# Kernel tuning notes

Hardware: AMD Instinct MI355X
Metric: run time of the kernel (lower is better)

Reference implementation:

```python
import jax, jax.numpy as jnp
import numpy as np

# task -> non-background class ids, padded with -1 to fixed width 3
NBG = np.array([[0, 1, 2], [0, 3, 4], [0, 5, 6], [0, 7, 8],
                [0, 9, -1], [0, 10, -1], [0, 11, -1]], dtype=np.int32)
NEG = -1e9      # pad logit (finite stand-in for -inf, grad-safe)
SMOOTH = 1e-5
NUM_CLASSES = 12


def setup_inputs() -> dict:
    key = jax.random.key(0)
    k1, k2, k3 = jax.random.split(key, 3)
    B, C, D, H, W = 4, 12, 32, 128, 128
    inputs = jax.random.normal(k1, (B, C, D, H, W), dtype=jnp.float32)
    task_id = jax.random.randint(k2, (B,), 0, 7, dtype=jnp.int32)
    # build targets consistent with each sample's task: labels in task_nbg[task]
    raw = jax.random.randint(k3, (B, D, H, W), 0, 3, dtype=jnp.int32)
    nbg = jnp.asarray(NBG)
    ids = nbg[task_id]                                   # [B,3]
    valid_max = jnp.where(ids[:, 2] < 0, 1, 2)           # 2-class tasks: raw in {0,1}
    raw = jnp.minimum(raw, valid_max[:, None, None, None])
    targets = jnp.take_along_axis(ids, raw.reshape(B, -1), axis=1).reshape(B, D, H, W)
    return {"inputs": inputs, "targets": targets, "task_id": task_id}


def reference(inputs, targets, task_id):
    B = inputs.shape[0]
    probs = jax.nn.softmax(inputs, axis=1)               # [B,12,D,H,W]
    nbg = jnp.asarray(NBG)
    ids = nbg[task_id]                                   # [B,3]
    mask = (ids >= 0)                                    # [B,3]
    idsc = jnp.maximum(ids, 0)
    mask5 = mask[:, :, None, None, None]
    gathered = jnp.take_along_axis(probs, idsc[:, :, None, None, None], axis=1)  # [B,3,D,H,W]
    score = jnp.where(mask5, gathered, 0.0)

    # --- remapped marginal targets: labels > 0 shifted by delta ---
    t = task_id.astype(jnp.int32)
    delta = jnp.where(t <= 4, -2 * t, -t - 4)
    tm = jnp.where(targets > 0, targets + delta[:, None, None, None], targets)   # in {0,1,2}

    # --- marginal CE: log_softmax over gathered probs (note: probs, not logits, matching torch F.cross_entropy on softmaxed inputs) ---
    logits = jnp.where(mask5, gathered, NEG)
    logp = jax.nn.log_softmax(logits, axis=1)
    nll = -jnp.take_along_axis(logp, tm[:, None], axis=1)[:, 0]                  # [B,D,H,W]
    loss_marg_ce = nll.mean(axis=(1, 2, 3)).sum() / B

    # --- marginal dice (padded classes contribute exactly 0) ---
    tgt = ((targets[:, None] == idsc[:, :, None, None, None]) & mask5).astype(probs.dtype)
    inter = jnp.sum(score * tgt, axis=(2, 3, 4))
    y_sum = jnp.sum(tgt, axis=(2, 3, 4))                 # tgt is binary: tgt*tgt == tgt
    z_sum = jnp.sum(score * score, axis=(2, 3, 4))
    dice = (2 * inter + SMOOTH) / (z_sum + y_sum + SMOOTH)
    loss_marg_dice = (1.0 - dice).sum() / B

    # --- exclusion: target_e = 1 - onehot(targets, 0..11), class 0 zeroed ---
    cls = jnp.arange(NUM_CLASSES, dtype=targets.dtype)[None, :, None, None, None]
    onehot = (targets[:, None] == cls).astype(probs.dtype)
    te = 1.0 - onehot
    te = te.at[:, 0].set(0.0)
    inter_e = jnp.sum(probs * te, axis=(2, 3, 4))
    y_e = jnp.sum(te, axis=(2, 3, 4))
    z_e = jnp.sum(probs * probs, axis=(2, 3, 4))
    dice_e = (2 * inter_e + SMOOTH) / (z_e + y_e + SMOOTH)
    loss_exc_dice = dice_e.sum() / B                     # inv=True: sum of dice scores

    loss_exc_ce = (jnp.log1p(probs) * te).mean(axis=(2, 3, 4)).sum() / B

    return (loss_marg_dice, loss_marg_ce, loss_exc_dice, loss_exc_ce)
```

## Files before the change

kernel.cpp:

```cpp
#include <hip/hip_runtime.h>


#define S2 262144
#define BLOCKS_PER_B 512
#define THREADS 256
#define ITERS 2
#define NVOX 524288.0f
#define SMOOTH 1e-5f

#define WRED(v) { v += __shfl_down(v,32); v += __shfl_down(v,16); \
                  v += __shfl_down(v,8);  v += __shfl_down(v,4);  \
                  v += __shfl_down(v,2);  v += __shfl_down(v,1); }

#define PROC2(X, TG, COMP) do {                                                \
  float xv[12];                                                                \
  _Pragma("unroll")                                                            \
  for (int c = 0; c < 12; ++c) xv[c] = X[c].COMP;                              \
  const int tgt = TG.COMP;                                                     \
  float m = xv[0];                                                             \
  _Pragma("unroll")                                                            \
  for (int c = 1; c < 12; ++c) m = fmaxf(m, xv[c]);                            \
  float e[12]; float es = 0.f;                                                 \
  _Pragma("unroll")                                                            \
  for (int c = 0; c < 12; ++c) { e[c] = __expf(xv[c] - m); es += e[c]; }       \
  const float r = __builtin_amdgcn_rcpf(es);                                   \
  float p[12];                                                                 \
  _Pragma("unroll")                                                            \
  for (int c = 0; c < 12; ++c) {                                               \
    p[c] = e[c] * r;                                                           \
    aZ[c] += p[c] * p[c];                                                      \
    aP[c] += p[c];                                                             \
  }                                                                            \
  float q = 1.f;                                                               \
  _Pragma("unroll")                                                            \
  for (int c = 1; c < 12; ++c) q = __builtin_fmaf(p[c], q, q);                 \
  const float g0 = p[0];                                                       \
  float g1 = 0.f, g2 = 0.f;                                                    \
  _Pragma("unroll")                                                            \
  for (int c = 1; c < 12; ++c) {                                               \
    if (c==1||c==3||c==5||c==7||c==9||c==10||c==11) g1 = (id1==c) ? p[c] : g1; \
    else                                            g2 = (id2==c) ? p[c] : g2; \
  }                                                                            \
  const bool t0 = (tgt == 0);                                                  \
  const bool t1 = (tgt == id1);                                                \
  const bool t2 = (tgt == id2);                                                \
  c0 += t0 ? 1.f : 0.f;  c1 += t1 ? 1.f : 0.f;  c2 += t2 ? 1.f : 0.f;          \
  p0S += t0 ? g0 : 0.f;  p1S += t1 ? g1 : 0.f;  p2S += t2 ? g2 : 0.f;          \
  const float pt = t1 ? g1 : (t2 ? g2 : 0.f);                                  \
  cesE += __logf(q * __builtin_amdgcn_rcpf(1.f + pt));                         \
  float s3 = __expf(g0) + __expf(g1);                                          \
  if (v2) s3 += __expf(g2);                                                    \
  const float gt = t0 ? g0 : (t1 ? g1 : g2);                                   \
  ces += __logf(s3) - gt;                                                      \
} while (0)

__global__ void zero_acc(float* __restrict__ acc) {
  acc[threadIdx.x] = 0.f;
}

__global__ __launch_bounds__(THREADS, 4)
void marg_main(const float2* __restrict__ inp, const int2* __restrict__ tgtp,
               const int* __restrict__ task_id, float* __restrict__ acc) {
  const int b   = blockIdx.x / BLOCKS_PER_B;
  const int blk = blockIdx.x % BLOCKS_PER_B;
  const int t   = task_id[b];
  const int id1 = (t <= 4) ? 2*t + 1 : t + 5;
  const int id2 = (t <= 3) ? 2*t + 2 : -1;
  const bool v2 = (id2 >= 0);

  const float2* inB = inp  + (size_t)b * 12 * S2;
  const int2*   tgB = tgtp + (size_t)b * S2;

  float aZ[12], aP[12];
  #pragma unroll
  for (int c = 0; c < 12; ++c) { aZ[c]=0.f; aP[c]=0.f; }
  float ces=0.f, cesE=0.f, c0=0.f, c1=0.f, c2=0.f, p0S=0.f, p1S=0.f, p2S=0.f;

  #pragma unroll 1
  for (int it = 0; it < ITERS; ++it) {
    const int s = blk * (ITERS * THREADS) + it * THREADS + (int)threadIdx.x;
    float2 x[12];
    #pragma unroll
    for (int c = 0; c < 12; ++c) x[c] = inB[c * S2 + s];
    const int2 tg = tgB[s];
    PROC2(x, tg, x); PROC2(x, tg, y);
  }

  WRED(ces); WRED(cesE); WRED(c0); WRED(c1); WRED(c2);
  WRED(p0S); WRED(p1S); WRED(p2S);
  #pragma unroll
  for (int c = 0; c < 12; ++c) { WRED(aZ[c]); WRED(aP[c]); }

  __shared__ float red[4][32];
  const int lane = threadIdx.x & 63;
  const int wv   = threadIdx.x >> 6;
  if (lane == 0) {
    float* rw = red[wv];
    rw[0]=ces; rw[1]=cesE; rw[2]=c0; rw[3]=c1; rw[4]=c2;
    rw[5]=p0S; rw[6]=p1S; rw[7]=p2S;
    #pragma unroll
    for (int c = 0; c < 12; ++c) { rw[8+c]=aZ[c]; rw[20+c]=aP[c]; }
  }
  __syncthreads();
  if (threadIdx.x < 32) {
    const float sv = red[0][threadIdx.x] + red[1][threadIdx.x]
                   + red[2][threadIdx.x] + red[3][threadIdx.x];
    atomicAdd(acc + b * 64 + threadIdx.x, sv);
  }
}

__global__ void finalize(const float* __restrict__ acc,
                         const int* __restrict__ task_id,
                         float* __restrict__ out) {
  if (threadIdx.x != 0) return;
  float lmd = 0.f, lmce = 0.f, led = 0.f, lece = 0.f;
  for (int b = 0; b < 4; ++b) {
    const float* a = acc + b * 64;
    const int t   = task_id[b];
    const int id1 = (t <= 4) ? 2*t + 1 : t + 5;
    const int id2 = (t <= 3) ? 2*t + 2 : -1;

    lmce += a[0] / NVOX;
    lece += a[1] / NVOX;

    const float d0 = (2.f*a[5] + SMOOTH) / (a[8 + 0]   + a[2] + SMOOTH);
    const float d1 = (2.f*a[6] + SMOOTH) / (a[8 + id1] + a[3] + SMOOTH);
    float d2 = 1.f;
    if (id2 >= 0)
      d2 = (2.f*a[7] + SMOOTH) / (a[8 + id2] + a[4] + SMOOTH);
    lmd += (1.f - d0) + (1.f - d1) + (1.f - d2);

    led += SMOOTH / (a[8] + SMOOTH);
    for (int c = 1; c < 12; ++c) {
      const float ptc  = (c == id1) ? a[6] : ((c == id2) ? a[7] : 0.f);
      const float cntc = (c == id1) ? a[3] : ((c == id2) ? a[4] : 0.f);
      const float inter = a[20 + c] - ptc;
      const float ye    = NVOX - cntc;
      led += (2.f*inter + SMOOTH) / (a[8 + c] + ye + SMOOTH);
    }
  }
  out[0] = lmd  * 0.25f;
  out[1] = lmce * 0.25f;
  out[2] = led  * 0.25f;
  out[3] = lece * 0.25f;
}

extern "C" void kernel_launch(void* const* d_in, const int* in_sizes, int n_in,
                              void* d_out, int out_size, void* d_ws, size_t ws_size,
                              hipStream_t stream) {
  const float* inputs  = (const float*)d_in[0];
  const int*   targets = (const int*)d_in[1];
  const int*   task_id = (const int*)d_in[2];
  float* out = (float*)d_out;
  float* acc = (float*)d_ws;

  zero_acc<<<1, 256, 0, stream>>>(acc);
  marg_main<<<dim3(4 * BLOCKS_PER_B), THREADS, 0, stream>>>(
      (const float2*)inputs, (const int2*)targets, task_id, acc);
  finalize<<<1, 64, 0, stream>>>(acc, task_id, out);
}
```

Measured before the change: 167.3 us.

## Stage input tiles through LDS with float4 loads per wave

Each block now loads its voxel tile cooperatively into shared memory with 16-byte float4 loads. Each wave loads three of the twelve class channels, and threads then read their voxels from LDS for the softmax and loss math. Before, every thread did twelve strided float2 global loads. The goal is wider, more efficient global memory transactions. In exchange it adds 24KB of LDS per block, extra syncthreads barriers, and a store/load round trip through shared memory, which may reduce occupancy and the overlap between loads and compute.

```diff
diff --git a/kernel.cpp b/kernel.cpp
--- a/kernel.cpp
+++ b/kernel.cpp
@@ -1,10 +1,11 @@
 #include <hip/hip_runtime.h>
 
 
-#define S2 262144
-#define BLOCKS_PER_B 512
 #define THREADS 256
-#define ITERS 2
+#define VOX_TILE 512
+#define PHASES 2
+#define TILES_PER_B 512
+#define S_TOT 524288
 #define NVOX 524288.0f
 #define SMOOTH 1e-5f
 
@@ -12,17 +13,14 @@
                   v += __shfl_down(v,8);  v += __shfl_down(v,4);  \
                   v += __shfl_down(v,2);  v += __shfl_down(v,1); }
 
-#define PROC2(X, TG, COMP) do {                                                \
-  float xv[12];                                                                \
+#define PROC(XV, TGT) do {                                                     \
+  const int tgt = (TGT);                                                       \
+  float m = XV[0];                                                             \
   _Pragma("unroll")                                                            \
-  for (int c = 0; c < 12; ++c) xv[c] = X[c].COMP;                              \
-  const int tgt = TG.COMP;                                                     \
-  float m = xv[0];                                                             \
-  _Pragma("unroll")                                                            \
-  for (int c = 1; c < 12; ++c) m = fmaxf(m, xv[c]);                            \
+  for (int c = 1; c < 12; ++c) m = fmaxf(m, XV[c]);                            \
   float e[12]; float es = 0.f;                                                 \
   _Pragma("unroll")                                                            \
-  for (int c = 0; c < 12; ++c) { e[c] = __expf(xv[c] - m); es += e[c]; }       \
+  for (int c = 0; c < 12; ++c) { e[c] = __expf(XV[c] - m); es += e[c]; }       \
   const float r = __builtin_amdgcn_rcpf(es);                                   \
   float p[12];                                                                 \
   _Pragma("unroll")                                                            \
@@ -59,17 +57,22 @@
 }
 
 __global__ __launch_bounds__(THREADS, 4)
-void marg_main(const float2* __restrict__ inp, const int2* __restrict__ tgtp,
+void marg_main(const float* __restrict__ inp, const int* __restrict__ tgtp,
                const int* __restrict__ task_id, float* __restrict__ acc) {
-  const int b   = blockIdx.x / BLOCKS_PER_B;
-  const int blk = blockIdx.x % BLOCKS_PER_B;
+  const int b    = blockIdx.x / TILES_PER_B;
+  const int tile = blockIdx.x % TILES_PER_B;
   const int t   = task_id[b];
   const int id1 = (t <= 4) ? 2*t + 1 : t + 5;
   const int id2 = (t <= 3) ? 2*t + 2 : -1;
   const bool v2 = (id2 >= 0);
 
-  const float2* inB = inp  + (size_t)b * 12 * S2;
-  const int2*   tgB = tgtp + (size_t)b * S2;
+  const float* inB = inp  + (size_t)b * 12 * S_TOT;
+  const int*   tgB = tgtp + (size_t)b * S_TOT;
+
+  __shared__ float ldsX[12][VOX_TILE];
+
+  const int lane = threadIdx.x & 63;
+  const int wv   = threadIdx.x >> 6;
 
   float aZ[12], aP[12];
   #pragma unroll
@@ -77,13 +80,29 @@
   float ces=0.f, cesE=0.f, c0=0.f, c1=0.f, c2=0.f, p0S=0.f, p1S=0.f, p2S=0.f;
 
   #pragma unroll 1
-  for (int it = 0; it < ITERS; ++it) {
-    const int s = blk * (ITERS * THREADS) + it * THREADS + (int)threadIdx.x;
-    float2 x[12];
+  for (int ph = 0; ph < PHASES; ++ph) {
+    const size_t vbase = ((size_t)tile * PHASES + ph) * VOX_TILE;
+    if (ph) __syncthreads();
     #pragma unroll
-    for (int c = 0; c < 12; ++c) x[c] = inB[c * S2 + s];
-    const int2 tg = tgB[s];
-    PROC2(x, tg, x); PROC2(x, tg, y);
+    for (int k = 0; k < 3; ++k) {
+      const int c = wv * 3 + k;
+      const float4* src = (const float4*)(inB + (size_t)c * S_TOT + vbase);
+      float4* dst = (float4*)(&ldsX[c][0]);
+      const float4 a0 = src[lane];
+      const float4 a1 = src[lane + 64];
+      dst[lane]      = a0;
+      dst[lane + 64] = a1;
+    }
+    __syncthreads();
+    #pragma unroll
+    for (int j = 0; j < 2; ++j) {
+      const int v = (int)threadIdx.x + j * 256;
+      const int tgv = tgB[vbase + v];
+      float xv[12];
+      #pragma unroll
+      for (int c = 0; c < 12; ++c) xv[c] = ldsX[c][v];
+      PROC(xv, tgv);
+    }
   }
 
   WRED(ces); WRED(cesE); WRED(c0); WRED(c1); WRED(c2);
@@ -92,8 +111,6 @@
   for (int c = 0; c < 12; ++c) { WRED(aZ[c]); WRED(aP[c]); }
 
   __shared__ float red[4][32];
-  const int lane = threadIdx.x & 63;
-  const int wv   = threadIdx.x >> 6;
   if (lane == 0) {
     float* rw = red[wv];
     rw[0]=ces; rw[1]=cesE; rw[2]=c0; rw[3]=c1; rw[4]=c2;
@@ -155,7 +172,7 @@
   float* acc = (float*)d_ws;
 
   zero_acc<<<1, 256, 0, stream>>>(acc);
-  marg_main<<<dim3(4 * BLOCKS_PER_B), THREADS, 0, stream>>>(
-      (const float2*)inputs, (const int2*)targets, task_id, acc);
+  marg_main<<<dim3(4 * TILES_PER_B), THREADS, 0, stream>>>(
+      inputs, targets, task_id, acc);
   finalize<<<1, 64, 0, stream>>>(acc, task_id, out);
 }
```

New measurement: 170.4 us. About the same (+1.8%).
